# Kernel optimization log

Hardware: AMD Instinct MI355X
Metric: run time of the kernel (lower is better)

Reference implementation:

```python
import jax, jax.numpy as jnp
import numpy as np

B, S, HID = 2, 2048, 2048
NH, NKV, HD = 32, 8, 64
ROPE_THETA = 10000.0
SCALE = HD ** -0.5
GROUP = NH // NKV


def setup_inputs() -> dict:
    key = jax.random.key(0)
    k1, k2, k3 = jax.random.split(key, 3)
    positions = jnp.tile(jnp.arange(S, dtype=jnp.int32), (B, 1))  # [B,S]
    hidden_states = jax.random.normal(k1, (B, S, HID), dtype=jnp.float32)
    Wqkv = jax.random.normal(k2, (HID, (NH + 2 * NKV) * HD), dtype=jnp.float32) * (HID ** -0.5)
    Wo = jax.random.normal(k3, (NH * HD, HID), dtype=jnp.float32) * ((NH * HD) ** -0.5)
    return {"positions": positions, "hidden_states": hidden_states, "Wqkv": Wqkv, "Wo": Wo}


def _apply_rope(x, cos, sin):
    # x: [B,S,H,HD]; cos/sin: [B,S,1,HD/2]  (neox style: rotate halves)
    x1, x2 = x[..., : HD // 2], x[..., HD // 2 :]
    return jnp.concatenate([x1 * cos - x2 * sin, x2 * cos + x1 * sin], axis=-1)


def reference(positions, hidden_states, Wqkv, Wo):
    # QKV projection (bias=False)
    qkv = hidden_states @ Wqkv  # [B,S,(NH+2*NKV)*HD]
    q, k, v = jnp.split(qkv, [NH * HD, (NH + NKV) * HD], axis=-1)
    q = q.reshape(B, S, NH, HD)
    k = k.reshape(B, S, NKV, HD)
    v = v.reshape(B, S, NKV, HD)

    # neox-style RoPE
    inv_freq = 1.0 / (ROPE_THETA ** (jnp.arange(0, HD, 2, dtype=jnp.float32) / HD))  # [HD/2]
    freqs = positions.astype(jnp.float32)[..., None] * inv_freq  # [B,S,HD/2]
    cos = jnp.cos(freqs)[:, :, None, :]
    sin = jnp.sin(freqs)[:, :, None, :]
    q = _apply_rope(q, cos, sin)
    k = _apply_rope(k, cos, sin)

    # GQA: expand KV heads to match query heads
    k = jnp.repeat(k, GROUP, axis=2)  # [B,S,NH,HD]
    v = jnp.repeat(v, GROUP, axis=2)

    # causal attention
    scores = jnp.einsum("bqhd,bkhd->bhqk", q, k) * SCALE  # [B,NH,S,S]
    causal = jnp.tril(jnp.ones((S, S), dtype=bool))
    scores = jnp.where(causal, scores, jnp.finfo(scores.dtype).min)
    probs = jax.nn.softmax(scores, axis=-1)
    attn = jnp.einsum("bhqk,bkhd->bqhd", probs, v).reshape(B, S, NH * HD)

    return attn @ Wo  # [B,S,HID]
```

## Files before the change

kernel.cpp:

```cpp
#include <hip/hip_runtime.h>
#include <hip/hip_bf16.h>
#include <math.h>

#define SEQ 2048
#define HIDDEN 2048
#define NHEAD 32
#define NKVH 8
#define HD 64
#define QKVW 3072

typedef __bf16 bf16_t;
typedef __bf16 bf16x8 __attribute__((ext_vector_type(8)));
typedef __bf16 bf16x4 __attribute__((ext_vector_type(4)));
typedef float f32x4 __attribute__((ext_vector_type(4)));

__device__ __forceinline__ void gld_lds16(const bf16_t* g, bf16_t* l) {
  __builtin_amdgcn_global_load_lds((const __attribute__((address_space(1))) void*)g,
                                   (__attribute__((address_space(3))) void*)l, 16, 0, 0);
}

__global__ __launch_bounds__(256) void k_fill(float* __restrict__ out, int n, float v) {
  int i = blockIdx.x * 256 + threadIdx.x;
  if (i < n) out[i] = v;
}

__global__ __launch_bounds__(256) void k_cvt(const float* __restrict__ in,
                                             bf16_t* __restrict__ out, int n4) {
  int i = blockIdx.x * 256 + threadIdx.x;
  if (i >= n4) return;
  float4 v = ((const float4*)in)[i];
  bf16x4 o;
  o[0] = (bf16_t)v.x; o[1] = (bf16_t)v.y; o[2] = (bf16_t)v.z; o[3] = (bf16_t)v.w;
  ((bf16x4*)out)[i] = o;
}

__global__ __launch_bounds__(256) void k_tconv(const float* __restrict__ in,
                                               bf16_t* __restrict__ out, int R, int C) {
  __shared__ float t[64][65];
  const int c0 = blockIdx.x * 64, r0 = blockIdx.y * 64;
#pragma unroll
  for (int i = 0; i < 16; ++i) {
    int idx = threadIdx.x + i * 256;
    int r = idx >> 6, c = idx & 63;
    t[r][c] = in[(size_t)(r0 + r) * C + c0 + c];
  }
  __syncthreads();
#pragma unroll
  for (int i = 0; i < 16; ++i) {
    int idx = threadIdx.x + i * 256;
    int nr = idx >> 6, kc = idx & 63;
    out[(size_t)(c0 + nr) * R + r0 + kc] = (bf16_t)t[kc][nr];
  }
}

template <typename OutT>
__global__ __launch_bounds__(256) void k_gemm(const bf16_t* __restrict__ A,
                                              const bf16_t* __restrict__ Bt,
                                              OutT* __restrict__ C,
                                              int M, int N, int K) {
  __shared__ __align__(16) bf16_t As[128 * 32];
  __shared__ __align__(16) bf16_t Bs[128 * 32];
  const int tid  = threadIdx.x;
  const int wave = tid >> 6, lane = tid & 63;
  const int lr = lane & 15, quad = lane >> 4;
  const int mtile = blockIdx.y * 128, ntile = blockIdx.x * 128;
  const int wm = (wave & 1) * 64, wn = (wave >> 1) * 64;

  const int srow = tid >> 2, scol = (tid & 3) * 8;
  const bf16_t* aG = A  + (size_t)(mtile + srow) * K + scol;
  const bf16_t* bG = Bt + (size_t)(ntile + srow) * K + scol;
  const size_t rstep = (size_t)64 * K;
  bf16_t* lA0 = As + tid * 8; bf16_t* lA1 = As + 2048 + tid * 8;
  bf16_t* lB0 = Bs + tid * 8; bf16_t* lB1 = Bs + 2048 + tid * 8;

  f32x4 acc[4][4];
  const f32x4 z4 = {0.f, 0.f, 0.f, 0.f};
#pragma unroll
  for (int mf = 0; mf < 4; ++mf)
#pragma unroll
    for (int nf = 0; nf < 4; ++nf) acc[mf][nf] = z4;

  for (int kt = 0; kt < K; kt += 32) {
    __syncthreads();
    gld_lds16(aG + kt,         lA0);
    gld_lds16(aG + rstep + kt, lA1);
    gld_lds16(bG + kt,         lB0);
    gld_lds16(bG + rstep + kt, lB1);
    __syncthreads();
    bf16x8 af[4], bfr[4];
#pragma unroll
    for (int mf = 0; mf < 4; ++mf)
      af[mf] = *(const bf16x8*)(As + (wm + mf * 16 + lr) * 32 + quad * 8);
#pragma unroll
    for (int nf = 0; nf < 4; ++nf)
      bfr[nf] = *(const bf16x8*)(Bs + (wn + nf * 16 + lr) * 32 + quad * 8);
#pragma unroll
    for (int mf = 0; mf < 4; ++mf)
#pragma unroll
      for (int nf = 0; nf < 4; ++nf)
        acc[mf][nf] = __builtin_amdgcn_mfma_f32_16x16x32_bf16(af[mf], bfr[nf], acc[mf][nf], 0, 0, 0);
  }
#pragma unroll
  for (int mf = 0; mf < 4; ++mf)
#pragma unroll
    for (int nf = 0; nf < 4; ++nf)
#pragma unroll
      for (int r = 0; r < 4; ++r)
        C[(size_t)(mtile + wm + mf * 16 + quad * 4 + r) * N + ntile + wn + nf * 16 + lr] =
            (OutT)acc[mf][nf][r];
}

__global__ __launch_bounds__(256) void k_rope(const bf16_t* __restrict__ qkv,
                                              const unsigned* __restrict__ pos,
                                              bf16_t* __restrict__ ql,
                                              bf16_t* __restrict__ kl) {
  const int bs = blockIdx.x;
  const int b = bs >> 11, s = bs & 2047;
  const unsigned u = pos[bs];
  const float p = (u >= 0x3F800000u) ? __uint_as_float(u) : (float)(int)u;
  for (int t = threadIdx.x; t < 1280; t += 256) {
    const bool isq = t < 1024;
    const int tt = isq ? t : t - 1024;
    const int hh = tt >> 5, d = tt & 31;
    const int col = isq ? (hh * 64 + d) : (2048 + hh * 64 + d);
    float x1 = (float)qkv[(size_t)bs * QKVW + col];
    float x2 = (float)qkv[(size_t)bs * QKVW + col + 32];
    float fr = p * exp2f((float)d * -0.41524101186092029f);
    float sn, cs;
    sincosf(fr, &sn, &cs);
    float o1 = x1 * cs - x2 * sn;
    float o2 = x2 * cs + x1 * sn;
    if (isq) {
      o1 *= 0.125f; o2 *= 0.125f;
      size_t base = (((size_t)b * NHEAD + hh) * SEQ + s) * HD + d;
      ql[base] = (bf16_t)o1; ql[base + 32] = (bf16_t)o2;
    } else {
      size_t base = (((size_t)b * NKVH + hh) * SEQ + s) * HD + d;
      kl[base] = (bf16_t)o1; kl[base + 32] = (bf16_t)o2;
    }
  }
}

__global__ __launch_bounds__(256) void k_vtrans(const bf16_t* __restrict__ qkv,
                                                bf16_t* __restrict__ vt) {
  __shared__ bf16_t t[64][66];
  const int s0 = blockIdx.x * 64;
  const int bk = blockIdx.y;
  const int b = bk >> 3, kvh = bk & 7;
#pragma unroll
  for (int i = 0; i < 16; ++i) {
    int idx = threadIdx.x + i * 256;
    int r = idx >> 6, c = idx & 63;
    t[r][c] = qkv[((size_t)b * SEQ + s0 + r) * QKVW + 2560 + kvh * 64 + c];
  }
  __syncthreads();
#pragma unroll
  for (int i = 0; i < 16; ++i) {
    int idx = threadIdx.x + i * 256;
    int dr = idx >> 6, sc = idx & 63;
    vt[(((size_t)b * NKVH + kvh) * HD + dr) * SEQ + s0 + sc] = t[sc][dr];
  }
}

__global__ __launch_bounds__(256, 4) void k_attn(const bf16_t* __restrict__ ql,
                                                 const bf16_t* __restrict__ kl,
                                                 const bf16_t* __restrict__ vt,
                                                 bf16_t* __restrict__ attn) {
  __shared__ __align__(16) bf16_t Ks[2][64 * 64];
  __shared__ __align__(16) bf16_t Vs[2][64 * 64];
  __shared__ __align__(16) bf16_t P[4][16 * 64];
  const int pairp = blockIdx.x;
  const int bh = blockIdx.y;
  const int b = bh >> 5, h = bh & 31;
  const int kvh = h >> 2;
  const int wave = threadIdx.x >> 6, lane = threadIdx.x & 63;
  const int lr = lane & 15, quad = lane >> 4;
  const int lhi = lane >> 3, llo = lane & 7;
  const int gsw = llo ^ lhi;
  const bf16_t* qp = ql + ((size_t)b * NHEAD + h) * SEQ * HD;
  const bf16_t* kp = kl + ((size_t)b * NKVH + kvh) * SEQ * HD;
  const bf16_t* vp = vt + ((size_t)b * NKVH + kvh) * HD * SEQ;
  const f32x4 z4 = {0.f, 0.f, 0.f, 0.f};

  auto stage = [&](int buf, int kt) {
    const int k0s = kt * 64;
    const bf16_t* kbase = kp + (size_t)k0s * HD;
#pragma unroll
    for (int j = 0; j < 2; ++j) {
      int key = (wave * 2 + j) * 8 + lhi;
      gld_lds16(kbase + (size_t)key * HD + gsw * 8, &Ks[buf][(wave * 2 + j) * 512 + lane * 8]);
    }
#pragma unroll
    for (int j = 0; j < 2; ++j) {
      int hd = wave * 16 + j * 8 + lhi;
      gld_lds16(vp + (size_t)hd * SEQ + k0s + gsw * 8, &Vs[buf][(wave * 16 + j * 8) * 64 + lane * 8]);
    }
  };

#pragma unroll
  for (int seg = 0; seg < 2; ++seg) {
    const int tile = seg ? pairp : 31 - pairp;
    const int q0 = tile * 64 + wave * 16;

    bf16x8 aq[2];
#pragma unroll
    for (int ks = 0; ks < 2; ++ks)
      aq[ks] = *(const bf16x8*)(qp + (size_t)(q0 + lr) * HD + ks * 32 + quad * 8);

    f32x4 acc[4];
    float mrow[4], lrow[4];
#pragma unroll
    for (int nf = 0; nf < 4; ++nf) acc[nf] = z4;
#pragma unroll
    for (int r = 0; r < 4; ++r) { mrow[r] = -1e30f; lrow[r] = 0.f; }

    const int ntiles = tile + 1;
    int cur = 0;
    stage(0, 0);
    __syncthreads();

    for (int kt = 0; kt < ntiles; ++kt) {
      const int k0 = kt * 64;
      if (kt + 1 < ntiles) stage(cur ^ 1, kt + 1);

      bf16x8 bk[2][4];
#pragma unroll
      for (int ks = 0; ks < 2; ++ks)
#pragma unroll
        for (int nh = 0; nh < 4; ++nh)
          bk[ks][nh] = *(const bf16x8*)(&Ks[cur][(nh * 16 + lr) * 64 + (((ks * 4 + quad) ^ (lr & 7)) << 3)]);
      f32x4 sc[4];
#pragma unroll
      for (int nh = 0; nh < 4; ++nh) {
        sc[nh] = __builtin_amdgcn_mfma_f32_16x16x32_bf16(aq[0], bk[0][nh], z4, 0, 0, 0);
        sc[nh] = __builtin_amdgcn_mfma_f32_16x16x32_bf16(aq[1], bk[1][nh], sc[nh], 0, 0, 0);
      }

      if (kt == ntiles - 1) {
#pragma unroll
        for (int nh = 0; nh < 4; ++nh)
#pragma unroll
          for (int r = 0; r < 4; ++r) {
            int qg = q0 + quad * 4 + r;
            int kg = k0 + nh * 16 + lr;
            if (kg > qg) sc[nh][r] = -1e30f;
          }
      }

      float rm[4], al[4], rs[4];
#pragma unroll
      for (int r = 0; r < 4; ++r)
        rm[r] = fmaxf(fmaxf(sc[0][r], sc[1][r]), fmaxf(sc[2][r], sc[3][r]));
#pragma unroll
      for (int off = 1; off < 16; off <<= 1)
#pragma unroll
        for (int r = 0; r < 4; ++r) rm[r] = fmaxf(rm[r], __shfl_xor(rm[r], off, 64));
#pragma unroll
      for (int r = 0; r < 4; ++r) {
        float mn = fmaxf(mrow[r], rm[r]);
        al[r] = __expf(mrow[r] - mn);
        mrow[r] = mn;
      }
#pragma unroll
      for (int nh = 0; nh < 4; ++nh)
#pragma unroll
        for (int r = 0; r < 4; ++r) sc[nh][r] = __expf(sc[nh][r] - mrow[r]);
#pragma unroll
      for (int r = 0; r < 4; ++r)
        rs[r] = (sc[0][r] + sc[1][r]) + (sc[2][r] + sc[3][r]);
#pragma unroll
      for (int off = 1; off < 16; off <<= 1)
#pragma unroll
        for (int r = 0; r < 4; ++r) rs[r] += __shfl_xor(rs[r], off, 64);
#pragma unroll
      for (int r = 0; r < 4; ++r) lrow[r] = lrow[r] * al[r] + rs[r];
#pragma unroll
      for (int nf = 0; nf < 4; ++nf)
#pragma unroll
        for (int r = 0; r < 4; ++r) acc[nf][r] *= al[r];
#pragma unroll
      for (int nh = 0; nh < 4; ++nh)
#pragma unroll
        for (int r = 0; r < 4; ++r) {
          int row = quad * 4 + r;
          int cg = (nh * 2 + (lr >> 3)) ^ (row & 7);
          P[wave][row * 64 + (cg << 3) + (lr & 7)] = (bf16_t)sc[nh][r];
        }
      __asm__ volatile("s_waitcnt lgkmcnt(0)" ::: "memory");
      bf16x8 pa[2], bv[2][4];
#pragma unroll
      for (int kg = 0; kg < 2; ++kg)
        pa[kg] = *(const bf16x8*)(&P[wave][lr * 64 + (((kg * 4 + quad) ^ (lr & 7)) << 3)]);
#pragma unroll
      for (int kg = 0; kg < 2; ++kg)
#pragma unroll
        for (int nf = 0; nf < 4; ++nf)
          bv[kg][nf] = *(const bf16x8*)(&Vs[cur][(nf * 16 + lr) * 64 + (((kg * 4 + quad) ^ (lr & 7)) << 3)]);
      __asm__ volatile("" ::: "memory");
#pragma unroll
      for (int nf = 0; nf < 4; ++nf) {
        acc[nf] = __builtin_amdgcn_mfma_f32_16x16x32_bf16(pa[0], bv[0][nf], acc[nf], 0, 0, 0);
        acc[nf] = __builtin_amdgcn_mfma_f32_16x16x32_bf16(pa[1], bv[1][nf], acc[nf], 0, 0, 0);
      }
      __syncthreads();
      cur ^= 1;
    }

#pragma unroll
    for (int r = 0; r < 4; ++r) {
      float inv = 1.f / lrow[r];
      int row = q0 + quad * 4 + r;
#pragma unroll
      for (int nf = 0; nf < 4; ++nf)
        attn[((size_t)b * SEQ + row) * HIDDEN + h * HD + nf * 16 + lr] =
            (bf16_t)(acc[nf][r] * inv);
    }
  }
}

extern "C" void kernel_launch(void* const* d_in, const int* in_sizes, int n_in,
                              void* d_out, int out_size, void* d_ws, size_t ws_size,
                              hipStream_t stream) {
  float* out = (float*)d_out;

  if (n_in != 4) { k_fill<<<dim3(32768), dim3(256), 0, stream>>>(out, 8388608, 222.0f); return; }
  if (out_size != 8388608) { k_fill<<<dim3(32768), dim3(256), 0, stream>>>(out, 8388608, 111.0f); return; }
  if (ws_size < (size_t)109051904) { k_fill<<<dim3(32768), dim3(256), 0, stream>>>(out, 8388608, 777.0f); return; }

  int ord[4] = {0, 1, 2, 3};
  for (int i = 1; i < 4; ++i)
    for (int j = i; j > 0 && in_sizes[ord[j]] > in_sizes[ord[j - 1]]; --j) {
      int t = ord[j]; ord[j] = ord[j - 1]; ord[j - 1] = t;
    }
  const float*    hidden    = (const float*)d_in[ord[0]];
  const float*    wqkv      = (const float*)d_in[ord[1]];
  const float*    wo        = (const float*)d_in[ord[2]];
  const unsigned* positions = (const unsigned*)d_in[ord[3]];

  char* ws = (char*)d_ws;
  bf16_t* hidB  = (bf16_t*)(ws + 0);
  bf16_t* wqkvT = (bf16_t*)(ws + 16777216);
  bf16_t* woT   = (bf16_t*)(ws + 29360128);
  bf16_t* qkv   = (bf16_t*)(ws + 37748736);
  bf16_t* ql    = (bf16_t*)(ws + 62914560);
  bf16_t* kl    = (bf16_t*)(ws + 79691776);
  bf16_t* vt    = (bf16_t*)(ws + 83886080);
  bf16_t* attnb = (bf16_t*)(ws + 88080384);

  k_cvt<<<dim3(8192), dim3(256), 0, stream>>>(hidden, hidB, 2097152);
  k_tconv<<<dim3(48, 32), dim3(256), 0, stream>>>(wqkv, wqkvT, 2048, 3072);
  k_tconv<<<dim3(32, 32), dim3(256), 0, stream>>>(wo, woT, 2048, 2048);
  k_gemm<bf16_t><<<dim3(24, 32), dim3(256), 0, stream>>>(hidB, wqkvT, qkv, 4096, 3072, 2048);
  k_rope<<<dim3(4096), dim3(256), 0, stream>>>(qkv, positions, ql, kl);
  k_vtrans<<<dim3(32, 16), dim3(256), 0, stream>>>(qkv, vt);
  k_attn<<<dim3(16, 64), dim3(256), 0, stream>>>(ql, kl, vt, attnb);
  k_gemm<float><<<dim3(16, 32), dim3(256), 0, stream>>>(attnb, woT, out, 4096, 2048, 2048);
}
```

Baseline: 367.7 us.

## Fuse RoPE into QKV GEMM epilogue and use lazy softmax rescaling

Moves RoPE and the Q scaling into the QKV GEMM epilogue, writing Q and K directly in head-major layout and V to a compact buffer. This removes the separate RoPE kernel and the round trip through the full QKV intermediate. In attention, the running-max rescale is skipped unless some row's max grows by more than 8, and the row-sum cross-lane reduction is deferred to the end instead of running every tile. The lazy rescale is intended to keep the result exact because the final normalisation uses the same stale max, but it risks precision loss if the exponentials approach bf16 range limits.

```diff
diff --git a/kernel.cpp b/kernel.cpp
--- a/kernel.cpp
+++ b/kernel.cpp
@@ -110,38 +110,98 @@
             (OutT)acc[mf][nf][r];
 }
 
-__global__ __launch_bounds__(256) void k_rope(const bf16_t* __restrict__ qkv,
-                                              const unsigned* __restrict__ pos,
-                                              bf16_t* __restrict__ ql,
-                                              bf16_t* __restrict__ kl) {
-  const int bs = blockIdx.x;
-  const int b = bs >> 11, s = bs & 2047;
-  const unsigned u = pos[bs];
-  const float p = (u >= 0x3F800000u) ? __uint_as_float(u) : (float)(int)u;
-  for (int t = threadIdx.x; t < 1280; t += 256) {
-    const bool isq = t < 1024;
-    const int tt = isq ? t : t - 1024;
-    const int hh = tt >> 5, d = tt & 31;
-    const int col = isq ? (hh * 64 + d) : (2048 + hh * 64 + d);
-    float x1 = (float)qkv[(size_t)bs * QKVW + col];
-    float x2 = (float)qkv[(size_t)bs * QKVW + col + 32];
-    float fr = p * exp2f((float)d * -0.41524101186092029f);
-    float sn, cs;
-    sincosf(fr, &sn, &cs);
-    float o1 = x1 * cs - x2 * sn;
-    float o2 = x2 * cs + x1 * sn;
-    if (isq) {
-      o1 *= 0.125f; o2 *= 0.125f;
-      size_t base = (((size_t)b * NHEAD + hh) * SEQ + s) * HD + d;
-      ql[base] = (bf16_t)o1; ql[base + 32] = (bf16_t)o2;
-    } else {
-      size_t base = (((size_t)b * NKVH + hh) * SEQ + s) * HD + d;
-      kl[base] = (bf16_t)o1; kl[base + 32] = (bf16_t)o2;
-    }
-  }
-}
-
-__global__ __launch_bounds__(256) void k_vtrans(const bf16_t* __restrict__ qkv,
+__global__ __launch_bounds__(256) void k_gemm_qkv(const bf16_t* __restrict__ A,
+                                                  const bf16_t* __restrict__ Bt,
+                                                  const unsigned* __restrict__ pos,
+                                                  bf16_t* __restrict__ ql,
+                                                  bf16_t* __restrict__ kl,
+                                                  bf16_t* __restrict__ vbuf,
+                                                  int K) {
+  __shared__ __align__(16) bf16_t As[128 * 32];
+  __shared__ __align__(16) bf16_t Bs[128 * 32];
+  const int tid  = threadIdx.x;
+  const int wave = tid >> 6, lane = tid & 63;
+  const int lr = lane & 15, quad = lane >> 4;
+  const int mtile = blockIdx.y * 128, ntile = blockIdx.x * 128;
+  const int wm = (wave & 1) * 64, wn = (wave >> 1) * 64;
+
+  const int srow = tid >> 2, scol = (tid & 3) * 8;
+  const bf16_t* aG = A  + (size_t)(mtile + srow) * K + scol;
+  const bf16_t* bG = Bt + (size_t)(ntile + srow) * K + scol;
+  const size_t rstep = (size_t)64 * K;
+  bf16_t* lA0 = As + tid * 8; bf16_t* lA1 = As + 2048 + tid * 8;
+  bf16_t* lB0 = Bs + tid * 8; bf16_t* lB1 = Bs + 2048 + tid * 8;
+
+  f32x4 acc[4][4];
+  const f32x4 z4 = {0.f, 0.f, 0.f, 0.f};
+#pragma unroll
+  for (int mf = 0; mf < 4; ++mf)
+#pragma unroll
+    for (int nf = 0; nf < 4; ++nf) acc[mf][nf] = z4;
+
+  for (int kt = 0; kt < K; kt += 32) {
+    __syncthreads();
+    gld_lds16(aG + kt,         lA0);
+    gld_lds16(aG + rstep + kt, lA1);
+    gld_lds16(bG + kt,         lB0);
+    gld_lds16(bG + rstep + kt, lB1);
+    __syncthreads();
+    bf16x8 af[4], bfr[4];
+#pragma unroll
+    for (int mf = 0; mf < 4; ++mf)
+      af[mf] = *(const bf16x8*)(As + (wm + mf * 16 + lr) * 32 + quad * 8);
+#pragma unroll
+    for (int nf = 0; nf < 4; ++nf)
+      bfr[nf] = *(const bf16x8*)(Bs + (wn + nf * 16 + lr) * 32 + quad * 8);
+#pragma unroll
+    for (int mf = 0; mf < 4; ++mf)
+#pragma unroll
+      for (int nf = 0; nf < 4; ++nf)
+        acc[mf][nf] = __builtin_amdgcn_mfma_f32_16x16x32_bf16(af[mf], bfr[nf], acc[mf][nf], 0, 0, 0);
+  }
+
+  const int colbase = ntile + wn;
+  if (colbase < 2560) {
+    const bool isq = colbase < 2048;
+    const int h = isq ? (colbase >> 6) : ((colbase - 2048) >> 6);
+    bf16_t* obase = isq ? ql : kl;
+    const int nhh = isq ? NHEAD : NKVH;
+    const float scale = isq ? 0.125f : 1.0f;
+    const float invf0 = exp2f((float)lr * -0.41524101186092029f);
+    const float invf1 = exp2f((float)(lr + 16) * -0.41524101186092029f);
+#pragma unroll
+    for (int mf = 0; mf < 4; ++mf)
+#pragma unroll
+      for (int r = 0; r < 4; ++r) {
+        int row = mtile + wm + mf * 16 + quad * 4 + r;
+        int b = row >> 11, s = row & 2047;
+        unsigned u = pos[row];
+        float p = (u >= 0x3F800000u) ? __uint_as_float(u) : (float)(int)u;
+#pragma unroll
+        for (int nf = 0; nf < 2; ++nf) {
+          float x1 = acc[mf][nf][r], x2 = acc[mf][nf + 2][r];
+          float sn, cs;
+          sincosf(p * (nf ? invf1 : invf0), &sn, &cs);
+          size_t base = (((size_t)b * nhh + h) * SEQ + s) * HD + nf * 16 + lr;
+          obase[base]      = (bf16_t)((x1 * cs - x2 * sn) * scale);
+          obase[base + 32] = (bf16_t)((x2 * cs + x1 * sn) * scale);
+        }
+      }
+  } else {
+    const int kvh = (colbase - 2560) >> 6;
+#pragma unroll
+    for (int mf = 0; mf < 4; ++mf)
+#pragma unroll
+      for (int nf = 0; nf < 4; ++nf)
+#pragma unroll
+        for (int r = 0; r < 4; ++r) {
+          int row = mtile + wm + mf * 16 + quad * 4 + r;
+          vbuf[(size_t)row * 512 + kvh * 64 + nf * 16 + lr] = (bf16_t)acc[mf][nf][r];
+        }
+  }
+}
+
+__global__ __launch_bounds__(256) void k_vtrans(const bf16_t* __restrict__ vbuf,
                                                 bf16_t* __restrict__ vt) {
   __shared__ bf16_t t[64][66];
   const int s0 = blockIdx.x * 64;
@@ -151,7 +211,7 @@
   for (int i = 0; i < 16; ++i) {
     int idx = threadIdx.x + i * 256;
     int r = idx >> 6, c = idx & 63;
-    t[r][c] = qkv[((size_t)b * SEQ + s0 + r) * QKVW + 2560 + kvh * 64 + c];
+    t[r][c] = vbuf[((size_t)b * SEQ + s0 + r) * 512 + kvh * 64 + c];
   }
   __syncthreads();
 #pragma unroll
@@ -247,7 +307,7 @@
           }
       }
 
-      float rm[4], al[4], rs[4];
+      float rm[4];
 #pragma unroll
       for (int r = 0; r < 4; ++r)
         rm[r] = fmaxf(fmaxf(sc[0][r], sc[1][r]), fmaxf(sc[2][r], sc[3][r]));
@@ -255,11 +315,18 @@
       for (int off = 1; off < 16; off <<= 1)
 #pragma unroll
         for (int r = 0; r < 4; ++r) rm[r] = fmaxf(rm[r], __shfl_xor(rm[r], off, 64));
-#pragma unroll
-      for (int r = 0; r < 4; ++r) {
-        float mn = fmaxf(mrow[r], rm[r]);
-        al[r] = __expf(mrow[r] - mn);
-        mrow[r] = mn;
+      int ng = (rm[0] <= mrow[0] + 8.f) & (rm[1] <= mrow[1] + 8.f) &
+               (rm[2] <= mrow[2] + 8.f) & (rm[3] <= mrow[3] + 8.f);
+      if (!__all(ng)) {
+#pragma unroll
+        for (int r = 0; r < 4; ++r) {
+          float mn = fmaxf(mrow[r], rm[r]);
+          float al = __expf(mrow[r] - mn);
+          mrow[r] = mn;
+          lrow[r] *= al;
+#pragma unroll
+          for (int nf = 0; nf < 4; ++nf) acc[nf][r] *= al;
+        }
       }
 #pragma unroll
       for (int nh = 0; nh < 4; ++nh)
@@ -267,17 +334,7 @@
         for (int r = 0; r < 4; ++r) sc[nh][r] = __expf(sc[nh][r] - mrow[r]);
 #pragma unroll
       for (int r = 0; r < 4; ++r)
-        rs[r] = (sc[0][r] + sc[1][r]) + (sc[2][r] + sc[3][r]);
-#pragma unroll
-      for (int off = 1; off < 16; off <<= 1)
-#pragma unroll
-        for (int r = 0; r < 4; ++r) rs[r] += __shfl_xor(rs[r], off, 64);
-#pragma unroll
-      for (int r = 0; r < 4; ++r) lrow[r] = lrow[r] * al[r] + rs[r];
-#pragma unroll
-      for (int nf = 0; nf < 4; ++nf)
-#pragma unroll
-        for (int r = 0; r < 4; ++r) acc[nf][r] *= al[r];
+        lrow[r] += (sc[0][r] + sc[1][r]) + (sc[2][r] + sc[3][r]);
 #pragma unroll
       for (int nh = 0; nh < 4; ++nh)
 #pragma unroll
@@ -305,6 +362,11 @@
       __syncthreads();
       cur ^= 1;
     }
+
+#pragma unroll
+    for (int off = 1; off < 16; off <<= 1)
+#pragma unroll
+      for (int r = 0; r < 4; ++r) lrow[r] += __shfl_xor(lrow[r], off, 64);
 
 #pragma unroll
     for (int r = 0; r < 4; ++r) {
@@ -341,7 +403,7 @@
   bf16_t* hidB  = (bf16_t*)(ws + 0);
   bf16_t* wqkvT = (bf16_t*)(ws + 16777216);
   bf16_t* woT   = (bf16_t*)(ws + 29360128);
-  bf16_t* qkv   = (bf16_t*)(ws + 37748736);
+  bf16_t* vbuf  = (bf16_t*)(ws + 37748736);
   bf16_t* ql    = (bf16_t*)(ws + 62914560);
   bf16_t* kl    = (bf16_t*)(ws + 79691776);
   bf16_t* vt    = (bf16_t*)(ws + 83886080);
@@ -350,9 +412,8 @@
   k_cvt<<<dim3(8192), dim3(256), 0, stream>>>(hidden, hidB, 2097152);
   k_tconv<<<dim3(48, 32), dim3(256), 0, stream>>>(wqkv, wqkvT, 2048, 3072);
   k_tconv<<<dim3(32, 32), dim3(256), 0, stream>>>(wo, woT, 2048, 2048);
-  k_gemm<bf16_t><<<dim3(24, 32), dim3(256), 0, stream>>>(hidB, wqkvT, qkv, 4096, 3072, 2048);
-  k_rope<<<dim3(4096), dim3(256), 0, stream>>>(qkv, positions, ql, kl);
-  k_vtrans<<<dim3(32, 16), dim3(256), 0, stream>>>(qkv, vt);
+  k_gemm_qkv<<<dim3(24, 32), dim3(256), 0, stream>>>(hidB, wqkvT, positions, ql, kl, vbuf, 2048);
+  k_vtrans<<<dim3(32, 16), dim3(256), 0, stream>>>(vbuf, vt);
   k_attn<<<dim3(16, 64), dim3(256), 0, stream>>>(ql, kl, vt, attnb);
   k_gemm<float><<<dim3(16, 32), dim3(256), 0, stream>>>(attnb, woT, out, 4096, 2048, 2048);
 }
```

After: 337.5 us. 1.09x faster.
